# Kernel optimization log

Measured on AMD Instinct MI355X. Metric: run time of the kernel, lower is better.

Reference implementation:

```python
import jax, jax.numpy as jnp
import numpy as np

NEG_SLOPE = 0.2


def gat_layer(x, src, dst, W, a_src, a_dst, num_nodes):
    """One PyG-style GATConv (self-loops already appended to src/dst).
    Returns [N, H, C] head-separated output (no bias/concat applied)."""
    H, C = a_src.shape
    h = (x @ W).reshape(num_nodes, H, C)            # [N,H,C]
    alpha_src = jnp.einsum('nhc,hc->nh', h, a_src)  # [N,H]
    alpha_dst = jnp.einsum('nhc,hc->nh', h, a_dst)  # [N,H]
    e = jax.nn.leaky_relu(alpha_src[src] + alpha_dst[dst], NEG_SLOPE)  # [E,H]
    # segment softmax over edges sharing the same destination node
    m = jax.ops.segment_max(e, dst, num_segments=num_nodes)[dst]
    ex = jnp.exp(e - m)
    denom = jax.ops.segment_sum(ex, dst, num_segments=num_nodes)[dst]
    alpha = ex / denom                               # [E,H]
    msg = h[src] * alpha[:, :, None]                 # [E,H,C]
    return jax.ops.segment_sum(msg, dst, num_segments=num_nodes)  # [N,H,C]


def setup_inputs() -> dict:
    key = jax.random.key(0)
    ks = jax.random.split(key, 10)
    N, E, IN, HID, OUT, H = 50000, 800000, 128, 32, 32, 4
    s = 0.1
    return {
        'x': jax.random.normal(ks[0], (N, IN), jnp.float32),
        'edge_index': jax.random.randint(ks[1], (2, E), 0, N, jnp.int64),
        'W1': jax.random.normal(ks[2], (IN, H * HID), jnp.float32) * s,
        'att_src1': jax.random.normal(ks[3], (H, HID), jnp.float32) * s,
        'att_dst1': jax.random.normal(ks[4], (H, HID), jnp.float32) * s,
        'b1': jax.random.normal(ks[5], (H * HID,), jnp.float32) * s,
        'W2': jax.random.normal(ks[6], (H * HID, OUT), jnp.float32) * s,
        'att_src2': jax.random.normal(ks[7], (1, OUT), jnp.float32) * s,
        'att_dst2': jax.random.normal(ks[8], (1, OUT), jnp.float32) * s,
        'b2': jax.random.normal(ks[9], (OUT,), jnp.float32) * s,
    }


def reference(x, edge_index, W1, att_src1, att_dst1, b1, W2, att_src2, att_dst2, b2):
    N = x.shape[0]
    # add self loops (PyG GATConv default)
    loop = jnp.arange(N, dtype=edge_index.dtype)
    src = jnp.concatenate([edge_index[0], loop])
    dst = jnp.concatenate([edge_index[1], loop])
    # layer 1: heads=4, concat=True
    h1 = gat_layer(x, src, dst, W1, att_src1, att_dst1, N).reshape(N, -1) + b1
    h1 = jax.nn.elu(h1)
    # layer 2: heads=1, concat=False -> mean over heads
    h2 = gat_layer(h1, src, dst, W2, att_src2, att_dst2, N).mean(axis=1) + b2
    return h2
```

## Files before the change

### kernel.cpp

```cpp
#include <hip/hip_runtime.h>
#include <math.h>

#define NEG_SLOPE 0.2f
typedef unsigned int uint;
typedef __attribute__((ext_vector_type(8))) short short8;
typedef __attribute__((ext_vector_type(4))) float floatx4;

__device__ __forceinline__ float lrelu(float x){ return x > 0.f ? x : NEG_SLOPE*x; }
__device__ __forceinline__ float sel4(float a,float b,float c,float d,int comp){
    return comp==0 ? a : (comp==1 ? b : (comp==2 ? c : d));
}
__device__ __forceinline__ uint f2bf(float f){
    uint u = __float_as_uint(f);
    return (u + 0x7FFFu + ((u>>16)&1u)) >> 16;
}
__device__ __forceinline__ float bf_lo(uint u){ return __uint_as_float(u<<16); }
__device__ __forceinline__ float bf_hi(uint u){ return __uint_as_float(u & 0xFFFF0000u); }
__device__ __forceinline__ float cexp(float x){ return __expf(fminf(x, 60.f)); }

__global__ __launch_bounds__(256) void k_prep(const float* __restrict__ W,
                                              ushort* __restrict__ wtb)
{
    int flat = blockIdx.x*1024 + threadIdx.x*4;
    int k = flat >> 7, c = flat & 127;
    float4 wv = *(const float4*)&W[flat];
    wtb[(size_t)(c+0)*128 + k] = (ushort)f2bf(wv.x);
    wtb[(size_t)(c+1)*128 + k] = (ushort)f2bf(wv.y);
    wtb[(size_t)(c+2)*128 + k] = (ushort)f2bf(wv.z);
    wtb[(size_t)(c+3)*128 + k] = (ushort)f2bf(wv.w);
}

__global__ __launch_bounds__(512) void k_g1b(const float* __restrict__ x,
    const ushort* __restrict__ wtb, uint* __restrict__ hb2, int N, int GB,
    const int* __restrict__ ei, int* __restrict__ bh, int E, int Etot, int NC, int NB)
{
    if (blockIdx.x >= GB){
        __shared__ uint hist[256];
        int c = blockIdx.x - GB;
        if (threadIdx.x < 256) hist[threadIdx.x] = 0;
        __syncthreads();
        int e0 = c*4096;
        #pragma unroll
        for (int r=0;r<8;r++){
            int e = e0 + r*512 + threadIdx.x;
            if (e < Etot){
                int d = (e < E) ? ei[E+e] : (e-E);
                atomicAdd(&hist[d>>8], 1u);
            }
        }
        __syncthreads();
        int b = threadIdx.x;
        if (b < NB) bh[(size_t)b*NC + c] = (int)hist[b];
        return;
    }
    __shared__ __align__(16) ushort xt[64][136];
    const int tid = threadIdx.x;
    const int row0 = blockIdx.x * 64;
    #pragma unroll
    for (int j=0;j<4;j++){
        int flat = j*2048 + tid*4;
        int r = flat >> 7, c = flat & 127;
        int gr = row0 + r;
        float4 xv = (gr < N) ? *(const float4*)&x[(size_t)gr*128 + c]
                             : make_float4(0.f,0.f,0.f,0.f);
        uint2 p;
        p.x = f2bf(xv.x) | (f2bf(xv.y)<<16);
        p.y = f2bf(xv.z) | (f2bf(xv.w)<<16);
        *(uint2*)&xt[r][c] = p;
    }
    __syncthreads();
    const int wv_ = tid >> 6, lane = tid & 63;
    const int l15 = lane & 15, hi = lane >> 4;
    const int rw = wv_ & 3, ch = wv_ >> 2;
    const int arow = rw*16 + l15;
    floatx4 acc[4];
    #pragma unroll
    for (int t=0;t<4;t++) acc[t] = (floatx4){0.f,0.f,0.f,0.f};
    #pragma unroll
    for (int ks=0; ks<4; ks++){
        short8 a = *(short8*)&xt[arow][ks*32 + hi*8];
        #pragma unroll
        for (int c4=0; c4<4; c4++){
            int ct = ch*4 + c4;
            short8 b = *(const short8*)&wtb[(size_t)(ct*16 + l15)*128 + ks*32 + hi*8];
            acc[c4] = __builtin_amdgcn_mfma_f32_16x16x32_bf16(a, b, acc[c4], 0, 0, 0);
        }
    }
    #pragma unroll
    for (int c4=0; c4<4; c4++){
        int ct = ch*4 + c4;
        #pragma unroll
        for (int r=0;r<4;r++){
            float v  = acc[c4][r];
            float pr = __shfl_xor(v, 1);
            int gr = row0 + rw*16 + (hi<<2) + r;
            if (((lane & 1) == 0) && gr < N)
                hb2[(size_t)gr*64 + ct*8 + (l15>>1)] = f2bf(v) | (f2bf(pr)<<16);
        }
    }
}

__global__ __launch_bounds__(256) void k_a1sc(const uint* __restrict__ hb2,
        const float* __restrict__ at_s, const float* __restrict__ at_d,
        float* __restrict__ as1, float* __restrict__ ad1, int N, int AB,
        const int* __restrict__ bh, int* __restrict__ bhs, int* __restrict__ partials2, int T)
{
    __shared__ int sm[256];
    if (blockIdx.x >= AB){
        int bid = blockIdx.x - AB;
        int tid = threadIdx.x;
        int i = bid*256 + tid;
        int v = (i < T) ? bh[i] : 0;
        sm[tid] = v;
        __syncthreads();
        for (int d=1; d<256; d<<=1){
            int t = (tid >= d) ? sm[tid-d] : 0;
            __syncthreads();
            sm[tid] += t;
            __syncthreads();
        }
        if (i < T) bhs[i] = sm[tid] - v;
        if (tid == 255) partials2[bid] = sm[255];
        return;
    }
    int wid = (blockIdx.x << 2) + (threadIdx.x >> 6);
    int lane = threadIdx.x & 63;
    if (wid >= N) return;
    uint hv = hb2[(size_t)wid*64 + lane];
    float f0 = bf_lo(hv), f1 = bf_hi(hv);
    float2 asv = *(const float2*)&at_s[2*lane];
    float2 adv = *(const float2*)&at_d[2*lane];
    float sa = f0*asv.x + f1*asv.y;
    float da = f0*adv.x + f1*adv.y;
    #pragma unroll
    for (int d=8; d>=1; d>>=1){ sa += __shfl_xor(sa,d); da += __shfl_xor(da,d); }
    if ((lane & 15) == 0){
        int head = lane >> 4;
        as1[(size_t)wid*4 + head] = sa;
        ad1[(size_t)wid*4 + head] = da;
    }
}

__global__ __launch_bounds__(256) void k_bscan23(int* __restrict__ bhs,
        const int* __restrict__ partials2, int nb2, int T)
{
    __shared__ int sm[256];
    int tid = threadIdx.x;
    int v = (tid < nb2) ? partials2[tid] : 0;
    sm[tid] = v;
    __syncthreads();
    for (int d=1; d<256; d<<=1){
        int t = (tid >= d) ? sm[tid-d] : 0;
        __syncthreads();
        sm[tid] += t;
        __syncthreads();
    }
    int boff = (blockIdx.x == 0) ? 0 : sm[blockIdx.x - 1];
    int i = blockIdx.x*256 + tid;
    if (i < T) bhs[i] += boff;
}

__global__ void k_bscan2s(int* __restrict__ bhs, const int* __restrict__ bh, int T){
    if (threadIdx.x == 0){
        int run = 0;
        for (int i=0;i<T;i++){ bhs[i] = run; run += bh[i]; }
    }
}

__global__ __launch_bounds__(256) void k_bscat(const int* __restrict__ ei,
        const int* __restrict__ bhs, uint* __restrict__ epack,
        int E, int Etot, int NC)
{
    __shared__ uint cnt[256];
    int c = blockIdx.x, tid = threadIdx.x;
    cnt[tid] = 0;
    __syncthreads();
    int e0 = c*4096;
    #pragma unroll
    for (int r=0;r<16;r++){
        int e = e0 + r*256 + tid;
        if (e < Etot){
            int d, s;
            if (e < E){ s = ei[e]; d = ei[E+e]; }
            else      { s = e - E; d = e - E; }
            int b = d >> 8;
            uint lr = atomicAdd(&cnt[b], 1u);
            int pos = bhs[(size_t)b*NC + c] + (int)lr;
            epack[pos] = (uint)s | ((uint)(d & 255) << 16);
        }
    }
}

__global__ __launch_bounds__(256) void k_bfin(const uint* __restrict__ epack,
        const int* __restrict__ bhs, int* __restrict__ bsrc,
        int* __restrict__ offs, int N, int NB, int NC, int Etot)
{
    __shared__ int cnt[256], lofs[256], cnt2[256], sm[256];
    int b = blockIdx.x, tid = threadIdx.x;
    int start = bhs[(size_t)b*NC];
    int end   = (b+1 < NB) ? bhs[(size_t)(b+1)*NC] : Etot;
    cnt[tid] = 0; cnt2[tid] = 0;
    __syncthreads();
    for (int e = start + tid; e < end; e += 256)
        atomicAdd((uint*)&cnt[(epack[e] >> 16) & 255], 1u);
    __syncthreads();
    int v = cnt[tid];
    sm[tid] = v;
    __syncthreads();
    for (int d=1; d<256; d<<=1){
        int t = (tid >= d) ? sm[tid-d] : 0;
        __syncthreads();
        sm[tid] += t;
        __syncthreads();
    }
    lofs[tid] = sm[tid] - v;
    int nd = b*256 + tid;
    if (nd <= N) offs[nd] = start + sm[tid] - v;
    __syncthreads();
    for (int e = start + tid; e < end; e += 256){
        uint u = epack[e];
        int dl = (u >> 16) & 255;
        int r = (int)atomicAdd((uint*)&cnt2[dl], 1u);
        bsrc[start + lofs[dl] + r] = (int)(u & 0xFFFFu);
    }
}

__global__ __launch_bounds__(256) void k_agg1(const uint* __restrict__ hb2,
    const float4* __restrict__ as1v, const float4* __restrict__ ad1v,
    const int* __restrict__ offs, const int* __restrict__ bsrc,
    const float* __restrict__ b1, float* __restrict__ exb,
    float* __restrict__ h1, int N)
{
    __shared__ float wsh[4][64][4];
    __shared__ int   ssh[4][64];
    int wv   = threadIdx.x >> 6;
    int wid  = (blockIdx.x << 2) + wv;
    int lane = threadIdx.x & 63;
    if (wid >= N) return;
    int base = offs[wid];
    int deg  = offs[wid+1] - base;
    float4 adv = ad1v[wid];
    const int comp = lane >> 4;
    float acc0=0.f, acc1=0.f;

    if (deg <= 64){
        const bool act = lane < deg;
        int sreg = 0;
        float e0=0.f,e1=0.f,e2=0.f,e3=0.f;
        if (act){
            sreg = bsrc[base+lane];
            float4 av = as1v[sreg];
            e0=cexp(lrelu(av.x+adv.x)); e1=cexp(lrelu(av.y+adv.y));
            e2=cexp(lrelu(av.z+adv.z)); e3=cexp(lrelu(av.w+adv.w));
        }
        float s0=e0,s1=e1,s2=e2,s3=e3;
        #pragma unroll
        for (int d=32; d>=1; d>>=1){
            s0+=__shfl_xor(s0,d); s1+=__shfl_xor(s1,d);
            s2+=__shfl_xor(s2,d); s3+=__shfl_xor(s3,d);
        }
        if (act){
            ssh[wv][lane]    = sreg << 6;
            wsh[wv][lane][0] = e0/s0;
            wsh[wv][lane][1] = e1/s1;
            wsh[wv][lane][2] = e2/s2;
            wsh[wv][lane][3] = e3/s3;
        }
        int j=0;
        for (; j+3 < deg; j+=4){
            uint oA=ssh[wv][j]+lane,   oB=ssh[wv][j+1]+lane;
            uint oC=ssh[wv][j+2]+lane, oD=ssh[wv][j+3]+lane;
            float wA=wsh[wv][j][comp],   wB=wsh[wv][j+1][comp];
            float wC=wsh[wv][j+2][comp], wD=wsh[wv][j+3][comp];
            uint hA=hb2[oA], hB=hb2[oB], hC=hb2[oC], hD=hb2[oD];
            acc0 = fmaf(bf_lo(hA), wA, acc0); acc1 = fmaf(bf_hi(hA), wA, acc1);
            acc0 = fmaf(bf_lo(hB), wB, acc0); acc1 = fmaf(bf_hi(hB), wB, acc1);
            acc0 = fmaf(bf_lo(hC), wC, acc0); acc1 = fmaf(bf_hi(hC), wC, acc1);
            acc0 = fmaf(bf_lo(hD), wD, acc0); acc1 = fmaf(bf_hi(hD), wD, acc1);
        }
        for (; j < deg; j++){
            uint oA = ssh[wv][j]+lane;
            float wA = wsh[wv][j][comp];
            uint hA = hb2[oA];
            acc0 = fmaf(bf_lo(hA), wA, acc0);
            acc1 = fmaf(bf_hi(hA), wA, acc1);
        }
    } else {
        float s0=0,s1=0,s2=0,s3=0;
        for (int j=lane; j<deg; j+=64){
            int s = bsrc[base+j];
            float4 av = as1v[s];
            float e0=cexp(lrelu(av.x+adv.x));
            float e1=cexp(lrelu(av.y+adv.y));
            float e2=cexp(lrelu(av.z+adv.z));
            float e3=cexp(lrelu(av.w+adv.w));
            s0+=e0; s1+=e1; s2+=e2; s3+=e3;
            *(float4*)&exb[(size_t)(base+j)*4] = make_float4(e0,e1,e2,e3);
        }
        #pragma unroll
        for (int d=32; d>=1; d>>=1){
            s0+=__shfl_xor(s0,d); s1+=__shfl_xor(s1,d);
            s2+=__shfl_xor(s2,d); s3+=__shfl_xor(s3,d);
        }
        float invc = 1.0f / sel4(s0,s1,s2,s3,comp);
        for (int j=0;j<deg;j++){
            int s = bsrc[base+j];
            float w = exb[(size_t)(base+j)*4 + comp]*invc;
            uint hv = hb2[((uint)s<<6)+lane];
            acc0 = fmaf(bf_lo(hv), w, acc0);
            acc1 = fmaf(bf_hi(hv), w, acc1);
        }
    }
    float2 bv = *(const float2*)&b1[2*lane];
    float r0 = acc0 + bv.x;
    float r1 = acc1 + bv.y;
    r0 = r0 > 0.f ? r0 : (__expf(r0) - 1.f);
    r1 = r1 > 0.f ? r1 : (__expf(r1) - 1.f);
    *(float2*)&h1[(size_t)wid*128 + 2*lane] = make_float2(r0, r1);
}

__global__ __launch_bounds__(256) void k_l2pre(const float* __restrict__ h1,
    const float* __restrict__ W2, const float* __restrict__ asrc2,
    const float* __restrict__ adst2, uint* __restrict__ h2b,
    float* __restrict__ as2, float* __restrict__ ad2, int N)
{
    __shared__ __align__(16) float w2s[4096];
    __shared__ float a2s[32], a2d[32];
    int tid = threadIdx.x;
    #pragma unroll
    for (int q=0;q<4;q++){
        int idx = q*1024 + tid*4;
        *(float4*)&w2s[idx] = *(const float4*)&W2[idx];
    }
    if (tid < 32){ a2s[tid] = asrc2[tid]; a2d[tid] = adst2[tid]; }
    __syncthreads();
    int node = blockIdx.x*8 + (tid>>5);
    if (node >= N) return;
    int c = tid & 31;
    float acc = 0.f;
    #pragma unroll 8
    for (int k=0;k<128;k+=4){
        float4 hv = *(const float4*)&h1[(size_t)node*128 + k];
        acc = fmaf(hv.x, w2s[(k+0)*32+c], acc);
        acc = fmaf(hv.y, w2s[(k+1)*32+c], acc);
        acc = fmaf(hv.z, w2s[(k+2)*32+c], acc);
        acc = fmaf(hv.w, w2s[(k+3)*32+c], acc);
    }
    float pr = __shfl_xor(acc, 1);
    if ((c & 1) == 0)
        h2b[(size_t)node*16 + (c>>1)] = f2bf(acc) | (f2bf(pr)<<16);
    float ps = acc * a2s[c], pd = acc * a2d[c];
    #pragma unroll
    for (int d=16; d>=1; d>>=1){ ps += __shfl_xor(ps,d); pd += __shfl_xor(pd,d); }
    if (c == 0){ as2[node] = ps; ad2[node] = pd; }
}

__global__ __launch_bounds__(256) void k_agg2(const uint* __restrict__ h2b,
    const float* __restrict__ as2, const float* __restrict__ ad2,
    const int* __restrict__ offs, const int* __restrict__ bsrc,
    const float* __restrict__ b2, float* __restrict__ exb,
    float* __restrict__ outp, int N)
{
    __shared__ float w2sh[4][64];
    __shared__ int   s2sh[4][64];
    int wv   = threadIdx.x >> 6;
    int wid  = (blockIdx.x << 2) + wv;
    int lane = threadIdx.x & 63;
    if (wid >= N) return;
    int base = offs[wid], deg = offs[wid+1] - base;
    float adn = ad2[wid];
    const int c2 = lane & 15, slot = lane >> 4;
    float acc0 = 0.f, acc1 = 0.f;

    if (deg <= 64){
        const bool act = lane < deg;
        int sreg = 0; float e = 0.f;
        if (act){ sreg = bsrc[base+lane]; e = cexp(lrelu(as2[sreg] + adn)); }
        float sum = e;
        #pragma unroll
        for (int d=32; d>=1; d>>=1) sum += __shfl_xor(sum,d);
        if (act){ s2sh[wv][lane] = sreg << 4; w2sh[wv][lane] = e/sum; }
        for (int j=slot; j<deg; j+=4){
            uint o  = (uint)(s2sh[wv][j] + c2);
            float w = w2sh[wv][j];
            uint u = h2b[o];
            acc0 = fmaf(bf_lo(u), w, acc0);
            acc1 = fmaf(bf_hi(u), w, acc1);
        }
    } else {
        float sum = 0.f;
        for (int j=lane; j<deg; j+=64){
            int s = bsrc[base+j];
            float ex = cexp(lrelu(as2[s] + adn));
            sum += ex;
            exb[base+j] = ex;
        }
        #pragma unroll
        for (int d=32; d>=1; d>>=1) sum += __shfl_xor(sum,d);
        float inv = 1.f/sum;
        for (int j=slot; j<deg; j+=4){
            int s  = bsrc[base+j];
            float w = exb[base+j]*inv;
            uint u = h2b[((uint)s<<4) + c2];
            acc0 = fmaf(bf_lo(u), w, acc0);
            acc1 = fmaf(bf_hi(u), w, acc1);
        }
    }
    acc0 += __shfl_xor(acc0, 16); acc0 += __shfl_xor(acc0, 32);
    acc1 += __shfl_xor(acc1, 16); acc1 += __shfl_xor(acc1, 32);
    if (lane < 16){
        float2 bv = *(const float2*)&b2[2*c2];
        *(float2*)&outp[(size_t)wid*32 + 2*c2] = make_float2(acc0 + bv.x, acc1 + bv.y);
    }
}

extern "C" void kernel_launch(void* const* d_in, const int* in_sizes, int n_in,
                              void* d_out, int out_size, void* d_ws, size_t ws_size,
                              hipStream_t stream)
{
    const float* x     = (const float*)d_in[0];
    const int*   ei    = (const int*)d_in[1];
    const float* W1    = (const float*)d_in[2];
    const float* at_s1 = (const float*)d_in[3];
    const float* at_d1 = (const float*)d_in[4];
    const float* b1    = (const float*)d_in[5];
    const float* W2    = (const float*)d_in[6];
    const float* at_s2 = (const float*)d_in[7];
    const float* at_d2 = (const float*)d_in[8];
    const float* b2    = (const float*)d_in[9];
    float* outp = (float*)d_out;

    const int N = in_sizes[0] / 128;
    const int E = in_sizes[1] / 2;
    const int Etot = E + N;

    const int NB = (N + 255) >> 8;
    const int NC = (Etot + 4095) / 4096;
    const int T  = NB * NC;
    const int L1 = (T + 255) / 256;

    float* f = (float*)d_ws;
    size_t off = 0;
    uint*  hb2 = (uint*)(f + off); off += (size_t)N*64;
    float* h1  = f + off; off += (size_t)N*128;
    float* exb = f + off; off += (size_t)Etot*4;
    float* as1 = f + off; off += (size_t)N*4;
    float* ad1 = f + off; off += (size_t)N*4;
    uint*  h2b = (uint*)(f + off); off += (size_t)N*16;
    float* as2 = f + off; off += (size_t)N;
    float* ad2 = f + off; off += (size_t)N;
    ushort* wtb = (ushort*)(f + off); off += 8192;
    int* ib       = (int*)(f + off);
    int* offs     = ib;
    int* bh       = ib + N + 8;
    int* bhs      = bh + T;
    int* partials2= bhs + T;
    uint* epack   = (uint*)(partials2 + 256);
    int* bsrc     = (int*)(epack + Etot);

    const int GB = (N+63)/64;
    const int AB = (N+3)/4;

    k_prep <<<16, 256, 0, stream>>>(W1, wtb);
    k_g1b  <<<GB+NC, 512, 0, stream>>>(x, wtb, hb2, N, GB, ei, bh, E, Etot, NC, NB);
    k_a1sc <<<AB+L1, 256, 0, stream>>>(hb2, at_s1, at_d1, as1, ad1, N, AB,
                                       bh, bhs, partials2, T);
    if (L1 <= 256){
        k_bscan23<<<L1, 256, 0, stream>>>(bhs, partials2, L1, T);
    } else {
        k_bscan2s<<<1, 1, 0, stream>>>(bhs, bh, T);
    }
    k_bscat<<<NC, 256, 0, stream>>>(ei, bhs, epack, E, Etot, NC);
    k_bfin <<<NB, 256, 0, stream>>>(epack, bhs, bsrc, offs, N, NB, NC, Etot);
    k_agg1 <<<(N+3)/4, 256, 0, stream>>>(hb2, (const float4*)as1, (const float4*)ad1,
                                         offs, bsrc, b1, exb, h1, N);
    k_l2pre<<<(N+7)/8, 256, 0, stream>>>(h1, W2, at_s2, at_d2, h2b, as2, ad2, N);
    k_agg2 <<<(N+3)/4, 256, 0, stream>>>(h2b, as2, ad2, offs, bsrc, b2, exb, outp, N);
}
```

Before: 162.1 us.

## Fuse block-scan pass into scatter/finalize, store layer-1 output as bf16, unroll gather

The separate k_bscan23 launch is removed. k_bscat and k_bfin now each redo the small partial-sum scan in shared memory and add the block offset themselves, and offs[N] is set in k_prep. The layer-1 activation h1 is written as packed bf16 instead of fp32, which halves the write in k_agg1 and the read in k_l2pre. The agg1 neighbour gather loop is also unrolled by 8 to keep more loads in flight. Together these cut one launch and some memory traffic, at the cost of redundant scan work per block and lower precision in h1.

```diff
diff --git a/kernel.cpp b/kernel.cpp
--- a/kernel.cpp
+++ b/kernel.cpp
@@ -19,8 +19,10 @@
 __device__ __forceinline__ float cexp(float x){ return __expf(fminf(x, 60.f)); }
 
 __global__ __launch_bounds__(256) void k_prep(const float* __restrict__ W,
-                                              ushort* __restrict__ wtb)
-{
+                                              ushort* __restrict__ wtb,
+                                              int* __restrict__ offs, int N, int Etot)
+{
+    if (blockIdx.x == 0 && threadIdx.x == 0) offs[N] = Etot;
     int flat = blockIdx.x*1024 + threadIdx.x*4;
     int k = flat >> 7, c = flat & 127;
     float4 wv = *(const float4*)&W[flat];
@@ -141,25 +143,6 @@
     }
 }
 
-__global__ __launch_bounds__(256) void k_bscan23(int* __restrict__ bhs,
-        const int* __restrict__ partials2, int nb2, int T)
-{
-    __shared__ int sm[256];
-    int tid = threadIdx.x;
-    int v = (tid < nb2) ? partials2[tid] : 0;
-    sm[tid] = v;
-    __syncthreads();
-    for (int d=1; d<256; d<<=1){
-        int t = (tid >= d) ? sm[tid-d] : 0;
-        __syncthreads();
-        sm[tid] += t;
-        __syncthreads();
-    }
-    int boff = (blockIdx.x == 0) ? 0 : sm[blockIdx.x - 1];
-    int i = blockIdx.x*256 + tid;
-    if (i < T) bhs[i] += boff;
-}
-
 __global__ void k_bscan2s(int* __restrict__ bhs, const int* __restrict__ bh, int T){
     if (threadIdx.x == 0){
         int run = 0;
@@ -168,11 +151,27 @@
 }
 
 __global__ __launch_bounds__(256) void k_bscat(const int* __restrict__ ei,
-        const int* __restrict__ bhs, uint* __restrict__ epack,
-        int E, int Etot, int NC)
-{
+        const int* __restrict__ bhs, const int* __restrict__ partials2, int L1e,
+        uint* __restrict__ epack, int E, int Etot, int NC, int NB)
+{
+    __shared__ int sm[256];
+    __shared__ int pbase[256];
     __shared__ uint cnt[256];
     int c = blockIdx.x, tid = threadIdx.x;
+    int v = (tid < L1e) ? partials2[tid] : 0;
+    sm[tid] = v;
+    __syncthreads();
+    for (int d=1; d<256; d<<=1){
+        int t = (tid >= d) ? sm[tid-d] : 0;
+        __syncthreads();
+        sm[tid] += t;
+        __syncthreads();
+    }
+    if (tid < NB){
+        int i = tid*NC + c;
+        int boff = (L1e == 0 || (i>>8) == 0) ? 0 : sm[(i>>8)-1];
+        pbase[tid] = bhs[i] + boff;
+    }
     cnt[tid] = 0;
     __syncthreads();
     int e0 = c*4096;
@@ -185,27 +184,42 @@
             else      { s = e - E; d = e - E; }
             int b = d >> 8;
             uint lr = atomicAdd(&cnt[b], 1u);
-            int pos = bhs[(size_t)b*NC + c] + (int)lr;
-            epack[pos] = (uint)s | ((uint)(d & 255) << 16);
+            epack[pbase[b] + (int)lr] = (uint)s | ((uint)(d & 255) << 16);
         }
     }
 }
 
 __global__ __launch_bounds__(256) void k_bfin(const uint* __restrict__ epack,
-        const int* __restrict__ bhs, int* __restrict__ bsrc,
-        int* __restrict__ offs, int N, int NB, int NC, int Etot)
-{
-    __shared__ int cnt[256], lofs[256], cnt2[256], sm[256];
+        const int* __restrict__ bhs, const int* __restrict__ partials2, int L1e,
+        int* __restrict__ bsrc, int* __restrict__ offs, int N, int NB, int NC, int Etot)
+{
+    __shared__ int sm[256];
+    __shared__ int cnt[256], lofs[256], cnt2[256];
     int b = blockIdx.x, tid = threadIdx.x;
-    int start = bhs[(size_t)b*NC];
-    int end   = (b+1 < NB) ? bhs[(size_t)(b+1)*NC] : Etot;
+    int v = (tid < L1e) ? partials2[tid] : 0;
+    sm[tid] = v;
+    __syncthreads();
+    for (int d=1; d<256; d<<=1){
+        int t = (tid >= d) ? sm[tid-d] : 0;
+        __syncthreads();
+        sm[tid] += t;
+        __syncthreads();
+    }
+    int i0 = b*NC;
+    int start = bhs[i0] + ((L1e==0 || (i0>>8)==0) ? 0 : sm[(i0>>8)-1]);
+    int end;
+    if (b+1 < NB){
+        int i1 = (b+1)*NC;
+        end = bhs[i1] + ((L1e==0 || (i1>>8)==0) ? 0 : sm[(i1>>8)-1]);
+    } else end = Etot;
+    __syncthreads();
     cnt[tid] = 0; cnt2[tid] = 0;
     __syncthreads();
     for (int e = start + tid; e < end; e += 256)
         atomicAdd((uint*)&cnt[(epack[e] >> 16) & 255], 1u);
     __syncthreads();
-    int v = cnt[tid];
-    sm[tid] = v;
+    int v2 = cnt[tid];
+    sm[tid] = v2;
     __syncthreads();
     for (int d=1; d<256; d<<=1){
         int t = (tid >= d) ? sm[tid-d] : 0;
@@ -213,9 +227,9 @@
         sm[tid] += t;
         __syncthreads();
     }
-    lofs[tid] = sm[tid] - v;
+    lofs[tid] = sm[tid] - v2;
     int nd = b*256 + tid;
-    if (nd <= N) offs[nd] = start + sm[tid] - v;
+    if (nd <= N) offs[nd] = start + sm[tid] - v2;
     __syncthreads();
     for (int e = start + tid; e < end; e += 256){
         uint u = epack[e];
@@ -229,7 +243,7 @@
     const float4* __restrict__ as1v, const float4* __restrict__ ad1v,
     const int* __restrict__ offs, const int* __restrict__ bsrc,
     const float* __restrict__ b1, float* __restrict__ exb,
-    float* __restrict__ h1, int N)
+    uint* __restrict__ hb1, int N)
 {
     __shared__ float wsh[4][64][4];
     __shared__ int   ssh[4][64];
@@ -267,6 +281,26 @@
             wsh[wv][lane][3] = e3/s3;
         }
         int j=0;
+        for (; j+7 < deg; j+=8){
+            uint o0=ssh[wv][j+0]+lane, o1=ssh[wv][j+1]+lane;
+            uint o2=ssh[wv][j+2]+lane, o3=ssh[wv][j+3]+lane;
+            uint o4=ssh[wv][j+4]+lane, o5=ssh[wv][j+5]+lane;
+            uint o6=ssh[wv][j+6]+lane, o7=ssh[wv][j+7]+lane;
+            float w0=wsh[wv][j+0][comp], w1=wsh[wv][j+1][comp];
+            float w2=wsh[wv][j+2][comp], w3=wsh[wv][j+3][comp];
+            float w4=wsh[wv][j+4][comp], w5=wsh[wv][j+5][comp];
+            float w6=wsh[wv][j+6][comp], w7=wsh[wv][j+7][comp];
+            uint h0=hb2[o0], h1_=hb2[o1], h2_=hb2[o2], h3=hb2[o3];
+            uint h4=hb2[o4], h5=hb2[o5], h6=hb2[o6], h7=hb2[o7];
+            acc0 = fmaf(bf_lo(h0), w0, acc0); acc1 = fmaf(bf_hi(h0), w0, acc1);
+            acc0 = fmaf(bf_lo(h1_),w1, acc0); acc1 = fmaf(bf_hi(h1_),w1, acc1);
+            acc0 = fmaf(bf_lo(h2_),w2, acc0); acc1 = fmaf(bf_hi(h2_),w2, acc1);
+            acc0 = fmaf(bf_lo(h3), w3, acc0); acc1 = fmaf(bf_hi(h3), w3, acc1);
+            acc0 = fmaf(bf_lo(h4), w4, acc0); acc1 = fmaf(bf_hi(h4), w4, acc1);
+            acc0 = fmaf(bf_lo(h5), w5, acc0); acc1 = fmaf(bf_hi(h5), w5, acc1);
+            acc0 = fmaf(bf_lo(h6), w6, acc0); acc1 = fmaf(bf_hi(h6), w6, acc1);
+            acc0 = fmaf(bf_lo(h7), w7, acc0); acc1 = fmaf(bf_hi(h7), w7, acc1);
+        }
         for (; j+3 < deg; j+=4){
             uint oA=ssh[wv][j]+lane,   oB=ssh[wv][j+1]+lane;
             uint oC=ssh[wv][j+2]+lane, oD=ssh[wv][j+3]+lane;
@@ -316,10 +350,10 @@
     float r1 = acc1 + bv.y;
     r0 = r0 > 0.f ? r0 : (__expf(r0) - 1.f);
     r1 = r1 > 0.f ? r1 : (__expf(r1) - 1.f);
-    *(float2*)&h1[(size_t)wid*128 + 2*lane] = make_float2(r0, r1);
-}
-
-__global__ __launch_bounds__(256) void k_l2pre(const float* __restrict__ h1,
+    hb1[(size_t)wid*64 + lane] = f2bf(r0) | (f2bf(r1)<<16);
+}
+
+__global__ __launch_bounds__(256) void k_l2pre(const uint* __restrict__ hb1,
     const float* __restrict__ W2, const float* __restrict__ asrc2,
     const float* __restrict__ adst2, uint* __restrict__ h2b,
     float* __restrict__ as2, float* __restrict__ ad2, int N)
@@ -338,13 +372,17 @@
     if (node >= N) return;
     int c = tid & 31;
     float acc = 0.f;
-    #pragma unroll 8
-    for (int k=0;k<128;k+=4){
-        float4 hv = *(const float4*)&h1[(size_t)node*128 + k];
-        acc = fmaf(hv.x, w2s[(k+0)*32+c], acc);
-        acc = fmaf(hv.y, w2s[(k+1)*32+c], acc);
-        acc = fmaf(hv.z, w2s[(k+2)*32+c], acc);
-        acc = fmaf(hv.w, w2s[(k+3)*32+c], acc);
+    #pragma unroll
+    for (int k=0;k<128;k+=8){
+        uint4 u = *(const uint4*)&hb1[(size_t)node*64 + (k>>1)];
+        acc = fmaf(bf_lo(u.x), w2s[(k+0)*32+c], acc);
+        acc = fmaf(bf_hi(u.x), w2s[(k+1)*32+c], acc);
+        acc = fmaf(bf_lo(u.y), w2s[(k+2)*32+c], acc);
+        acc = fmaf(bf_hi(u.y), w2s[(k+3)*32+c], acc);
+        acc = fmaf(bf_lo(u.z), w2s[(k+4)*32+c], acc);
+        acc = fmaf(bf_hi(u.z), w2s[(k+5)*32+c], acc);
+        acc = fmaf(bf_lo(u.w), w2s[(k+6)*32+c], acc);
+        acc = fmaf(bf_hi(u.w), w2s[(k+7)*32+c], acc);
     }
     float pr = __shfl_xor(acc, 1);
     if ((c & 1) == 0)
@@ -442,7 +480,7 @@
     float* f = (float*)d_ws;
     size_t off = 0;
     uint*  hb2 = (uint*)(f + off); off += (size_t)N*64;
-    float* h1  = f + off; off += (size_t)N*128;
+    uint*  hb1 = (uint*)(f + off); off += (size_t)N*64;
     float* exb = f + off; off += (size_t)Etot*4;
     float* as1 = f + off; off += (size_t)N*4;
     float* ad1 = f + off; off += (size_t)N*4;
@@ -461,19 +499,20 @@
     const int GB = (N+63)/64;
     const int AB = (N+3)/4;
 
-    k_prep <<<16, 256, 0, stream>>>(W1, wtb);
+    k_prep <<<16, 256, 0, stream>>>(W1, wtb, offs, N, Etot);
     k_g1b  <<<GB+NC, 512, 0, stream>>>(x, wtb, hb2, N, GB, ei, bh, E, Etot, NC, NB);
     k_a1sc <<<AB+L1, 256, 0, stream>>>(hb2, at_s1, at_d1, as1, ad1, N, AB,
                                        bh, bhs, partials2, T);
     if (L1 <= 256){
-        k_bscan23<<<L1, 256, 0, stream>>>(bhs, partials2, L1, T);
+        k_bscat<<<NC, 256, 0, stream>>>(ei, bhs, partials2, L1, epack, E, Etot, NC, NB);
+        k_bfin <<<NB, 256, 0, stream>>>(epack, bhs, partials2, L1, bsrc, offs, N, NB, NC, Etot);
     } else {
         k_bscan2s<<<1, 1, 0, stream>>>(bhs, bh, T);
-    }
-    k_bscat<<<NC, 256, 0, stream>>>(ei, bhs, epack, E, Etot, NC);
-    k_bfin <<<NB, 256, 0, stream>>>(epack, bhs, bsrc, offs, N, NB, NC, Etot);
+        k_bscat<<<NC, 256, 0, stream>>>(ei, bhs, partials2, 0, epack, E, Etot, NC, NB);
+        k_bfin <<<NB, 256, 0, stream>>>(epack, bhs, partials2, 0, bsrc, offs, N, NB, NC, Etot);
+    }
     k_agg1 <<<(N+3)/4, 256, 0, stream>>>(hb2, (const float4*)as1, (const float4*)ad1,
-                                         offs, bsrc, b1, exb, h1, N);
-    k_l2pre<<<(N+7)/8, 256, 0, stream>>>(h1, W2, at_s2, at_d2, h2b, as2, ad2, N);
+                                         offs, bsrc, b1, exb, hb1, N);
+    k_l2pre<<<(N+7)/8, 256, 0, stream>>>(hb1, W2, at_s2, at_d2, h2b, as2, ad2, N);
     k_agg2 <<<(N+3)/4, 256, 0, stream>>>(h2b, as2, ad2, offs, bsrc, b2, exb, outp, N);
 }
```

New measurement: 146.1 us. 9.9% less time.
